# Performance work log

Hardware: AMD Instinct MI355X
Metric: run time of the kernel (lower is better)

The kernel has to match this reference:

```python
import jax, jax.numpy as jnp
import numpy as np

# (C,H,W) of x0..x11; flattened size +1 homogeneous coordinate per key
SHAPES = [(3,32,32),(96,32,32),(96,32,32),(96,16,16),(192,16,16),(192,16,16),(192,8,8),(192,8,8),(192,8,8),(640,1,1),(100,1,1),(10,1,1)]
# (Cin,Cout,k,stride,pad) for conv1..conv9
CONV = [(3,96,3,1,1),(96,96,3,1,1),(96,96,3,2,1),(96,192,3,1,1),(192,192,3,1,1),(192,192,3,2,1),(192,192,3,1,1),(192,192,1,1,0),(192,10,1,1,0)]
B = 128


def setup_inputs():
    key = jax.random.key(0)
    inp = {}
    k, key = jax.random.split(key)
    inp['x0'] = jax.random.normal(k, (int(np.prod(SHAPES[0])) + 1, B), jnp.float32)
    for i, s in enumerate(SHAPES):
        n = int(np.prod(s)) + 1
        k1, k2, key = jax.random.split(key, 3)
        inp['perm%d' % i] = jax.random.permutation(k1, n)
        inp['diag%d' % i] = jax.random.uniform(k2, (n,), jnp.float32, 0.5, 1.5)
    for j, (ci, co, ks, st, pd) in enumerate(CONV):
        k1, k2, key = jax.random.split(key, 3)
        inp['w%d' % (j + 1)] = jax.random.normal(k1, (co, ci, ks, ks), jnp.float32) / np.float32(np.sqrt(ci * ks * ks))
        inp['b%d' % (j + 1)] = jax.random.normal(k2, (co,), jnp.float32) * 0.01
    k1, k2, k3, k4 = jax.random.split(key, 4)
    inp['fw1'] = jax.random.normal(k1, (100, 640), jnp.float32) / np.float32(np.sqrt(640))
    inp['fb1'] = jax.random.normal(k2, (100,), jnp.float32) * 0.01
    inp['fw2'] = jax.random.normal(k3, (10, 100), jnp.float32) / np.float32(np.sqrt(100))
    inp['fb2'] = jax.random.normal(k4, (10,), jnp.float32) * 0.01
    return inp


def _decode(x, perm, diag):
    # A_inv @ x with A_inv = P^T D^{-1}; P^T gather index is argsort(perm)
    return (x / diag[:, None])[jnp.argsort(perm)]


def _encode(y, perm, diag):
    # A @ y with A = D P; (P y)[i] = y[perm[i]]
    return diag[:, None] * y[perm]


def _conv_aug(v, w, b, shape_in, stride, pad):
    # affine-augmented conv: [W b; 0 1] applied to [feat; t]
    C, H, Wd = shape_in
    feat, t = v[:-1], v[-1]                      # (C*H*W, B), (B,)
    x = feat.T.reshape(-1, C, H, Wd)
    y = jax.lax.conv_general_dilated(x, w, (stride, stride), [(pad, pad), (pad, pad)],
                                     dimension_numbers=('NCHW', 'OIHW', 'NCHW'))
    y = y + b[None, :, None, None] * t[:, None, None, None]
    yf = y.reshape(y.shape[0], -1).T             # (N_out, B)
    return jnp.concatenate([yf, t[None, :]], axis=0)


def _fc_aug(v, w, b):
    feat, t = v[:-1], v[-1]
    return jnp.concatenate([w @ feat + b[:, None] * t[None, :], t[None, :]], axis=0)


def _forward(x0, perms, diags, ws, bs, fw1, fb1, fw2, fb2):
    x = x0
    for i in range(9):
        v = _decode(x, perms[i], diags[i])
        y = _conv_aug(v, ws[i], bs[i], SHAPES[i], CONV[i][3], CONV[i][4])
        x = jax.nn.relu(_encode(y, perms[i + 1], diags[i + 1]))
    v = _decode(x, perms[9], diags[9])
    x = jax.nn.relu(_encode(_fc_aug(v, fw1, fb1), perms[10], diags[10]))
    v = _decode(x, perms[10], diags[10])
    return _encode(_fc_aug(v, fw2, fb2), perms[11], diags[11])


def reference(x0, perm0, perm1, perm2, perm3, perm4, perm5, perm6, perm7, perm8, perm9, perm10, perm11,
              diag0, diag1, diag2, diag3, diag4, diag5, diag6, diag7, diag8, diag9, diag10, diag11,
              w1, b1, w2, b2, w3, b3, w4, b4, w5, b5, w6, b6, w7, b7, w8, b8, w9, b9,
              fw1, fb1, fw2, fb2):
    perms = [perm0, perm1, perm2, perm3, perm4, perm5, perm6, perm7, perm8, perm9, perm10, perm11]
    diags = [diag0, diag1, diag2, diag3, diag4, diag5, diag6, diag7, diag8, diag9, diag10, diag11]
    ws = [w1, w2, w3, w4, w5, w6, w7, w8, w9]
    bs = [b1, b2, b3, b4, b5, b6, b7, b8, b9]
    return _forward(x0, perms, diags, ws, bs, fw1, fb1, fw2, fb2)
```

## Files before the change

kernel.cpp:

```cpp
#include <hip/hip_runtime.h>


#define B 128
#define ZPAD 2048

typedef _Float16 f16_t;
typedef __attribute__((ext_vector_type(8))) _Float16 f16x8;
typedef __attribute__((ext_vector_type(4))) _Float16 f16x4;
typedef __attribute__((ext_vector_type(4))) float f32x4;


__global__ void decode_kernel(const float* __restrict__ x, const int* __restrict__ perm,
                              const float* __restrict__ diag, float* __restrict__ v, int nrows) {
    int row = blockIdx.x * 8 + (threadIdx.x >> 5);
    if (row >= nrows) return;
    int lane = threadIdx.x & 31;
    int p = perm[row];
    float inv = 1.0f / diag[row];
    float4 val = ((const float4*)(x + (size_t)row * B))[lane];
    val.x *= inv; val.y *= inv; val.z *= inv; val.w *= inv;
    ((float4*)(v + (size_t)p * B))[lane] = val;
}

__global__ void encode_kernel(const float* __restrict__ y, const int* __restrict__ perm,
                              const float* __restrict__ diag, float* __restrict__ out, int nrows) {
    int row = blockIdx.x * 8 + (threadIdx.x >> 5);
    if (row >= nrows) return;
    int lane = threadIdx.x & 31;
    int p = perm[row];
    float d = diag[row];
    float4 val = ((const float4*)(y + (size_t)p * B))[lane];
    val.x *= d; val.y *= d; val.z *= d; val.w *= d;
    ((float4*)(out + (size_t)row * B))[lane] = val;
}

__global__ void fc_kernel(const float* __restrict__ v, const float* __restrict__ w,
                          const float* __restrict__ b, float* __restrict__ y,
                          int K, int R, int do_relu) {
    int r = blockIdx.x;
    int n = threadIdx.x;
    float t = v[(size_t)K * B + n];
    float val;
    if (r == R) {
        val = t;
    } else {
        float a0 = 0.f, a1 = 0.f, a2 = 0.f, a3 = 0.f;
        float a4 = 0.f, a5 = 0.f, a6 = 0.f, a7 = 0.f;
        const float* wr = w + (size_t)r * K;
        int k = 0;
        for (; k + 8 <= K; k += 8) {
            float4 w0 = *(const float4*)(wr + k);
            float4 w1 = *(const float4*)(wr + k + 4);
            float x0 = v[(size_t)(k + 0) * B + n];
            float x1 = v[(size_t)(k + 1) * B + n];
            float x2 = v[(size_t)(k + 2) * B + n];
            float x3 = v[(size_t)(k + 3) * B + n];
            float x4 = v[(size_t)(k + 4) * B + n];
            float x5 = v[(size_t)(k + 5) * B + n];
            float x6 = v[(size_t)(k + 6) * B + n];
            float x7 = v[(size_t)(k + 7) * B + n];
            a0 = fmaf(w0.x, x0, a0);
            a1 = fmaf(w0.y, x1, a1);
            a2 = fmaf(w0.z, x2, a2);
            a3 = fmaf(w0.w, x3, a3);
            a4 = fmaf(w1.x, x4, a4);
            a5 = fmaf(w1.y, x5, a5);
            a6 = fmaf(w1.z, x6, a6);
            a7 = fmaf(w1.w, x7, a7);
        }
        for (; k < K; ++k)
            a0 = fmaf(wr[k], v[(size_t)k * B + n], a0);
        val = b[r] * t + ((a0 + a1) + (a2 + a3)) + ((a4 + a5) + (a6 + a7));
    }
    if (do_relu) val = fmaxf(val, 0.f);
    y[(size_t)r * B + n] = val;
}


__global__ void pack_input_kernel(const float* __restrict__ v, f16_t* __restrict__ xout,
                                  float* __restrict__ tout) {
    int idx = blockIdx.x * 256 + threadIdx.x;
    int p = idx >> 7, n = idx & 127;
    f16x8 o = {};
    o[0] = (f16_t)v[(size_t)(0 * 1024 + p) * B + n];
    o[1] = (f16_t)v[(size_t)(1 * 1024 + p) * B + n];
    o[2] = (f16_t)v[(size_t)(2 * 1024 + p) * B + n];
    *(f16x8*)(xout + ZPAD + (size_t)p * 1024 + n * 8) = o;
    if (idx < B) tout[idx] = v[(size_t)3072 * B + idx];
}


struct WArgs {
    const float* w[9]; const float* b[9];
    int Ci[9], Co[9], KS[9], Cp[9], NCG[9];
    int woff[10]; int boff[10];
};

__global__ void pack_weights_kernel(WArgs A, f16_t* __restrict__ wp, float* __restrict__ bp,
                                    f16_t* __restrict__ x8a, f16_t* __restrict__ x8b) {
    int idx = blockIdx.x * 256 + threadIdx.x;
    if (idx < ZPAD) { x8a[idx] = (f16_t)0.f; x8b[idx] = (f16_t)0.f; }
    if (idx < A.boff[9]) {
        int l = 0;
        while (idx >= A.boff[l + 1]) ++l;
        int co = idx - A.boff[l];
        bp[idx] = (co < A.Co[l]) ? A.b[l][co] : 0.f;
    }
    if (idx >= A.woff[9]) return;
    int l = 0;
    while (idx >= A.woff[l + 1]) ++l;
    int e = idx - A.woff[l];
    int j = e & 7;
    int t1 = e >> 3;
    int Cp = A.Cp[l];
    int co = t1 % Cp;
    int gg = t1 / Cp;
    int ncg = A.NCG[l];
    int tap = gg / ncg, cg = gg - tap * ncg;
    int ks = A.KS[l];
    int kh = tap / ks, kw = tap - kh * ks;
    int ci = cg * 8 + j;
    float val = 0.f;
    if (co < A.Co[l] && tap < ks * ks && ci < A.Ci[l])
        val = A.w[l][(((size_t)co * A.Ci[l] + ci) * ks + kh) * ks + kw];
    wp[idx] = (f16_t)val;
}


template <int KS, int NS, int NSPLIT, bool F32OUT>
__global__ __launch_bounds__(64) void conv_mfma_kernel(
    const f16_t* __restrict__ xin, const float* __restrict__ t_in,
    const f16_t* __restrict__ wp, const float* __restrict__ bp,
    f16_t* __restrict__ xout, float* __restrict__ t_out, float* __restrict__ f32out,
    int Hi, int Wi, int Wo_log2, int HWo,
    int stride, int pad, int NCG, int nchunk, int KGr, int Co, int Co_pad,
    int PB8, int CB)
{
    constexpr int PF = 2;
    constexpr int MS = 4;
    const int lane = threadIdx.x;
    const int q = lane >> 4;
    const int r = lane & 15;

    const int gb = blockIdx.x;
    const int xcd = gb & 7;
    int j = gb >> 3;
    int nh = 0;
    if (NSPLIT == 2) { nh = j & 1; j >>= 1; }
    const int cog = j % CB;
    const int p   = xcd * PB8 + j / CB;
    const int co0 = cog * 64;
    const int ncol0 = nh * (NS * 16);
    const int ncol8 = ncol0 * 8;

    const int ho = p >> Wo_log2;
    const int wo = p & ((1 << Wo_log2) - 1);
    const f16_t* xdata = xin + ZPAD;

    float tv[NS];
#pragma unroll
    for (int ns = 0; ns < NS; ++ns) tv[ns] = t_in[ncol0 + ns * 16 + r];

    f32x4 acc[MS][NS];
#pragma unroll
    for (int ms = 0; ms < MS; ++ms) {
        float4 b4 = *(const float4*)(bp + co0 + ms * 16 + q * 4);
#pragma unroll
        for (int ns = 0; ns < NS; ++ns) {
            acc[ms][ns][0] = b4.x * tv[ns];
            acc[ms][ns][1] = b4.y * tv[ns];
            acc[ms][ns][2] = b4.z * tv[ns];
            acc[ms][ns][3] = b4.w * tv[ns];
        }
    }

    const int hb = ho * stride - pad, wb = wo * stride - pad;
    const int HiWi = Hi * Wi;
    const int HiWi4 = 4 * HiWi;
    const int NCGHW = NCG * HiWi;
    const int wend = wb + KS;

    int g = q, cg = q, hi = hb, wi = wb, cgHW;
    {
        while (cg >= NCG) { cg -= NCG; ++wi; if (wi == wend) { wi = wb; ++hi; } }
        cgHW = cg * HiWi;
    }

    f16x8 bf[PF][NS], af[PF][MS];

    auto advance = [&]() {
        g += 4; cg += 4; cgHW += HiWi4;
        if (NCG >= 4) {
            int c2 = cg - NCG;
            bool wrap = c2 >= 0;
            int wn = wi + 1;
            bool ww = wrap & (wn == wend);
            cg   = wrap ? c2 : cg;
            cgHW = wrap ? cgHW - NCGHW : cgHW;
            wi   = wrap ? (ww ? wb : wn) : wi;
            hi   = ww ? hi + 1 : hi;
        } else {
            while (cg >= NCG) { cg -= NCG; cgHW -= NCGHW; ++wi; if (wi == wend) { wi = wb; ++hi; } }
        }
    };
    auto loadB = [&](f16x8* b) {
        bool v = (g < KGr) & ((unsigned)hi < (unsigned)Hi) & ((unsigned)wi < (unsigned)Wi);
        int boff = (cgHW + hi * Wi + wi) << 10;
        const f16_t* bb = xdata + (v ? boff : -ZPAD) + ncol8 + r * 8;
#pragma unroll
        for (int ns = 0; ns < NS; ++ns) b[ns] = *(const f16x8*)(bb + ns * 128);
    };
    auto loadA = [&](f16x8* a, int c) {
        int ac = c < nchunk ? c : nchunk - 1;
        const f16_t* ap = wp + (((ac * 4 + q) * Co_pad) + co0 + r) * 8;
#pragma unroll
        for (int ms = 0; ms < MS; ++ms) a[ms] = *(const f16x8*)(ap + ms * 128);
    };
    auto domfma = [&](f16x8* a, f16x8* b) {
#pragma unroll
        for (int ms = 0; ms < MS; ++ms)
#pragma unroll
            for (int ns = 0; ns < NS; ++ns)
                acc[ms][ns] = __builtin_amdgcn_mfma_f32_16x16x32_f16(a[ms], b[ns], acc[ms][ns], 0, 0, 0);
    };

#pragma unroll
    for (int pf = 0; pf < PF; ++pf) { loadB(bf[pf]); loadA(af[pf], pf); advance(); }
    const int nck = ((nchunk + PF - 1) / PF) * PF;
    for (int c = 0; c < nck; c += PF) {
#pragma unroll
        for (int pf = 0; pf < PF; ++pf) {
            domfma(af[pf], bf[pf]);
            loadB(bf[pf]); loadA(af[pf], c + PF + pf); advance();
        }
    }

    if (!F32OUT) {
#pragma unroll
        for (int ms = 0; ms < MS; ++ms) {
            int cob = co0 + ms * 16 + q * 4;
            if (cob < Co) {
                int off0 = ((cob >> 3) * HWo + p) * 1024 + (cob & 7) + ncol8 + r * 8;
#pragma unroll
                for (int ns = 0; ns < NS; ++ns) {
                    f16x4 h;
                    h[0] = (f16_t)fmaxf(acc[ms][ns][0], 0.f);
                    h[1] = (f16_t)fmaxf(acc[ms][ns][1], 0.f);
                    h[2] = (f16_t)fmaxf(acc[ms][ns][2], 0.f);
                    h[3] = (f16_t)fmaxf(acc[ms][ns][3], 0.f);
                    *(f16x4*)(xout + ZPAD + off0 + ns * 128) = h;
                }
            }
        }
        if (gb == 0) {
            t_out[lane]      = fmaxf(t_in[lane], 0.f);
            t_out[lane + 64] = fmaxf(t_in[lane + 64], 0.f);
        }
    } else {
#pragma unroll
        for (int ms = 0; ms < MS; ++ms)
#pragma unroll
            for (int ns = 0; ns < NS; ++ns)
#pragma unroll
                for (int e = 0; e < 4; ++e) {
                    int co = co0 + ms * 16 + q * 4 + e;
                    if (co < Co)
                        f32out[((size_t)co * HWo + p) * B + ncol0 + ns * 16 + r] =
                            fmaxf(acc[ms][ns][e], 0.f);
                }
        if (gb == 0) {
            f32out[(size_t)Co * HWo * B + lane]      = fmaxf(t_in[lane], 0.f);
            f32out[(size_t)Co * HWo * B + lane + 64] = fmaxf(t_in[lane + 64], 0.f);
        }
    }
}


extern "C" void kernel_launch(void* const* d_in, const int* in_sizes, int n_in,
                              void* d_out, int out_size, void* d_ws, size_t ws_size,
                              hipStream_t stream) {
    const float* x0 = (const float*)d_in[0];
    const int*   perm[12];
    const float* diag[12];
    for (int i = 0; i < 12; ++i) {
        perm[i] = (const int*)d_in[1 + 2 * i];
        diag[i] = (const float*)d_in[2 + 2 * i];
    }
    const float* wts[9];
    const float* bia[9];
    for (int j = 0; j < 9; ++j) {
        wts[j] = (const float*)d_in[25 + 2 * j];
        bia[j] = (const float*)d_in[26 + 2 * j];
    }
    const float* fw1 = (const float*)d_in[43];
    const float* fb1 = (const float*)d_in[44];
    const float* fw2 = (const float*)d_in[45];
    const float* fb2 = (const float*)d_in[46];
    float* out = (float*)d_out;

    static const int CiA[9]  = {3, 96, 96, 96, 192, 192, 192, 192, 192};
    static const int CoA[9]  = {96, 96, 96, 192, 192, 192, 192, 192, 10};
    static const int KSA[9]  = {3, 3, 3, 3, 3, 3, 3, 1, 1};
    static const int CpA[9]  = {128, 128, 128, 192, 192, 192, 192, 192, 64};
    static const int NCGA[9] = {1, 12, 12, 12, 24, 24, 24, 24, 24};
    static const int KGRA[9] = {9, 108, 108, 108, 216, 216, 216, 24, 24};
    static const int NCHK[9] = {3, 27, 27, 27, 54, 54, 54, 6, 6};
    static const int HiA[9]  = {32, 32, 32, 16, 16, 16, 8, 8, 8};
    static const int WoL[9]  = {5, 5, 4, 4, 4, 3, 3, 3, 3};
    static const int HWoA[9] = {1024, 1024, 256, 256, 256, 64, 64, 64, 64};
    static const int STA[9]  = {1, 1, 2, 1, 1, 2, 1, 1, 1};
    static const int PDA[9]  = {1, 1, 1, 1, 1, 1, 1, 0, 0};
    static const int NSPL[9] = {1, 1, 1, 1, 1, 2, 2, 2, 2};

    char* wsb = (char*)d_ws;
    const size_t BUF_F32  = 1574912;
    const size_t X8_BYTES = (size_t)(ZPAD + 12 * 1024 * 1024) * 2;
    float* bufA = (float*)wsb;
    float* bufB = (float*)(wsb + BUF_F32);
    f16_t* x8a  = (f16_t*)(wsb + 2 * BUF_F32);
    f16_t* x8b  = (f16_t*)(wsb + 2 * BUF_F32 + X8_BYTES);
    f16_t* wpb  = (f16_t*)(wsb + 2 * BUF_F32 + 2 * X8_BYTES);
    const size_t WP_BYTES = 2888704;
    float* bpb  = (float*)(wsb + 2 * BUF_F32 + 2 * X8_BYTES + WP_BYTES);
    float* t0   = (float*)((char*)bpb + 8192);
    float* t1   = t0 + 256;

    WArgs WA;
    int wo = 0, bo = 0;
    for (int l = 0; l < 9; ++l) {
        WA.w[l] = wts[l]; WA.b[l] = bia[l];
        WA.Ci[l] = CiA[l]; WA.Co[l] = CoA[l]; WA.KS[l] = KSA[l];
        WA.Cp[l] = CpA[l]; WA.NCG[l] = NCGA[l];
        WA.woff[l] = wo; wo += NCHK[l] * 4 * CpA[l] * 8;
        WA.boff[l] = bo; bo += CpA[l];
    }
    WA.woff[9] = wo; WA.boff[9] = bo;
    pack_weights_kernel<<<(wo + 255) / 256, 256, 0, stream>>>(WA, wpb, bpb, x8a, x8b);

    decode_kernel<<<(3073 + 7) / 8, 256, 0, stream>>>(x0, perm[0], diag[0], bufA, 3073);
    pack_input_kernel<<<131072 / 256, 256, 0, stream>>>(bufA, x8a, t0);

    f16_t* xin = x8a; f16_t* xout = x8b;
    float* tin = t0;  float* tout = t1;
    for (int l = 0; l < 9; ++l) {
        const int PB8 = HWoA[l] / 8;
        const int CB = CpA[l] / 64;
        dim3 grid(8 * PB8 * CB * NSPL[l]);
        const f16_t* wpl = wpb + WA.woff[l];
        const float* bpl = bpb + WA.boff[l];
        if (l <= 4) {
            conv_mfma_kernel<3, 8, 1, false><<<grid, 64, 0, stream>>>(
                xin, tin, wpl, bpl, xout, tout, nullptr,
                HiA[l], HiA[l], WoL[l], HWoA[l], STA[l], PDA[l],
                NCGA[l], NCHK[l], KGRA[l], CoA[l], CpA[l], PB8, CB);
        } else if (l <= 6) {
            conv_mfma_kernel<3, 4, 2, false><<<grid, 64, 0, stream>>>(
                xin, tin, wpl, bpl, xout, tout, nullptr,
                HiA[l], HiA[l], WoL[l], HWoA[l], STA[l], PDA[l],
                NCGA[l], NCHK[l], KGRA[l], CoA[l], CpA[l], PB8, CB);
        } else if (l == 7) {
            conv_mfma_kernel<1, 4, 2, false><<<grid, 64, 0, stream>>>(
                xin, tin, wpl, bpl, xout, tout, nullptr,
                HiA[l], HiA[l], WoL[l], HWoA[l], STA[l], PDA[l],
                NCGA[l], NCHK[l], KGRA[l], CoA[l], CpA[l], PB8, CB);
        } else {
            conv_mfma_kernel<1, 4, 2, true><<<grid, 64, 0, stream>>>(
                xin, tin, wpl, bpl, nullptr, nullptr, bufA,
                HiA[l], HiA[l], WoL[l], HWoA[l], STA[l], PDA[l],
                NCGA[l], NCHK[l], KGRA[l], CoA[l], CpA[l], PB8, CB);
        }
        f16_t* xt = xin; xin = xout; xout = xt;
        float* tt = tin; tin = tout; tout = tt;
    }

    fc_kernel<<<101, B, 0, stream>>>(bufA, fw1, fb1, bufB, 640, 100, 1);
    fc_kernel<<<11, B, 0, stream>>>(bufB, fw2, fb2, bufA, 100, 10, 0);
    encode_kernel<<<2, 256, 0, stream>>>(bufA, perm[11], diag[11], out, 11);
}
```

Before: 336.5 us.

## Merge output-channel blocks into multi-wave workgroups and fuse fc2 with encode

For conv layers 1-5, each workgroup now holds one wave per 64-channel output block (2 or 3 waves) covering the same pixel. Before, separate single-wave blocks each handled one channel block. The intent is to share input tile loads across waves through cache and cut the block count. The final FC layer and the encode permutation/scale are also fused into one kernel, which removes one launch and an intermediate buffer round-trip. The trade-off is fewer, larger blocks, which may reduce parallelism on a many-CU GPU.

```diff
diff --git a/kernel.cpp b/kernel.cpp
--- a/kernel.cpp
+++ b/kernel.cpp
@@ -20,18 +20,6 @@
     float4 val = ((const float4*)(x + (size_t)row * B))[lane];
     val.x *= inv; val.y *= inv; val.z *= inv; val.w *= inv;
     ((float4*)(v + (size_t)p * B))[lane] = val;
-}
-
-__global__ void encode_kernel(const float* __restrict__ y, const int* __restrict__ perm,
-                              const float* __restrict__ diag, float* __restrict__ out, int nrows) {
-    int row = blockIdx.x * 8 + (threadIdx.x >> 5);
-    if (row >= nrows) return;
-    int lane = threadIdx.x & 31;
-    int p = perm[row];
-    float d = diag[row];
-    float4 val = ((const float4*)(y + (size_t)p * B))[lane];
-    val.x *= d; val.y *= d; val.z *= d; val.w *= d;
-    ((float4*)(out + (size_t)row * B))[lane] = val;
 }
 
 __global__ void fc_kernel(const float* __restrict__ v, const float* __restrict__ w,
@@ -76,6 +64,32 @@
     y[(size_t)r * B + n] = val;
 }
 
+__global__ void fc2_encode_kernel(const float* __restrict__ v, const float* __restrict__ w,
+                                  const float* __restrict__ b, const int* __restrict__ perm,
+                                  const float* __restrict__ diag, float* __restrict__ out) {
+    int jrow = blockIdx.x;
+    int n = threadIdx.x;
+    int r = perm[jrow];
+    float d = diag[jrow];
+    float t = v[100 * B + n];
+    float val;
+    if (r == 10) {
+        val = t;
+    } else {
+        float a0 = 0.f, a1 = 0.f, a2 = 0.f, a3 = 0.f;
+        const float* wr = w + (size_t)r * 100;
+        for (int k = 0; k < 100; k += 4) {
+            float4 w4 = *(const float4*)(wr + k);
+            a0 = fmaf(w4.x, v[(size_t)(k + 0) * B + n], a0);
+            a1 = fmaf(w4.y, v[(size_t)(k + 1) * B + n], a1);
+            a2 = fmaf(w4.z, v[(size_t)(k + 2) * B + n], a2);
+            a3 = fmaf(w4.w, v[(size_t)(k + 3) * B + n], a3);
+        }
+        val = b[r] * t + (a0 + a1) + (a2 + a3);
+    }
+    out[(size_t)jrow * B + n] = d * val;
+}
+
 
 __global__ void pack_input_kernel(const float* __restrict__ v, f16_t* __restrict__ xout,
                                   float* __restrict__ tout) {
@@ -127,8 +141,8 @@
 }
 
 
-template <int KS, int NS, int NSPLIT, bool F32OUT>
-__global__ __launch_bounds__(64) void conv_mfma_kernel(
+template <int KS, int NS, int NSPLIT, int CBW, bool F32OUT>
+__global__ __launch_bounds__(64 * CBW) void conv_mfma_kernel(
     const f16_t* __restrict__ xin, const float* __restrict__ t_in,
     const f16_t* __restrict__ wp, const float* __restrict__ bp,
     f16_t* __restrict__ xout, float* __restrict__ t_out, float* __restrict__ f32out,
@@ -138,17 +152,23 @@
 {
     constexpr int PF = 2;
     constexpr int MS = 4;
-    const int lane = threadIdx.x;
+    const int wave = threadIdx.x >> 6;
+    const int lane = threadIdx.x & 63;
     const int q = lane >> 4;
     const int r = lane & 15;
 
     const int gb = blockIdx.x;
     const int xcd = gb & 7;
     int j = gb >> 3;
-    int nh = 0;
-    if (NSPLIT == 2) { nh = j & 1; j >>= 1; }
-    const int cog = j % CB;
-    const int p   = xcd * PB8 + j / CB;
+    int nh = 0, cog, p;
+    if (CBW > 1) {
+        cog = wave;
+        p = xcd * PB8 + j;
+    } else {
+        if (NSPLIT == 2) { nh = j & 1; j >>= 1; }
+        cog = j % CB;
+        p = xcd * PB8 + j / CB;
+    }
     const int co0 = cog * 64;
     const int ncol0 = nh * (NS * 16);
     const int ncol8 = ncol0 * 8;
@@ -253,8 +273,8 @@
             }
         }
         if (gb == 0) {
-            t_out[lane]      = fmaxf(t_in[lane], 0.f);
-            t_out[lane + 64] = fmaxf(t_in[lane + 64], 0.f);
+            for (int i = threadIdx.x; i < B; i += CBW * 64)
+                t_out[i] = fmaxf(t_in[i], 0.f);
         }
     } else {
 #pragma unroll
@@ -269,8 +289,8 @@
                             fmaxf(acc[ms][ns][e], 0.f);
                 }
         if (gb == 0) {
-            f32out[(size_t)Co * HWo * B + lane]      = fmaxf(t_in[lane], 0.f);
-            f32out[(size_t)Co * HWo * B + lane + 64] = fmaxf(t_in[lane + 64], 0.f);
+            for (int i = threadIdx.x; i < B; i += CBW * 64)
+                f32out[(size_t)Co * HWo * B + i] = fmaxf(t_in[i], 0.f);
         }
     }
 }
@@ -345,26 +365,30 @@
     for (int l = 0; l < 9; ++l) {
         const int PB8 = HWoA[l] / 8;
         const int CB = CpA[l] / 64;
-        dim3 grid(8 * PB8 * CB * NSPL[l]);
         const f16_t* wpl = wpb + WA.woff[l];
         const float* bpl = bpb + WA.boff[l];
-        if (l <= 4) {
-            conv_mfma_kernel<3, 8, 1, false><<<grid, 64, 0, stream>>>(
+        if (l <= 2) {
+            conv_mfma_kernel<3, 8, 1, 2, false><<<8 * PB8, 128, 0, stream>>>(
+                xin, tin, wpl, bpl, xout, tout, nullptr,
+                HiA[l], HiA[l], WoL[l], HWoA[l], STA[l], PDA[l],
+                NCGA[l], NCHK[l], KGRA[l], CoA[l], CpA[l], PB8, CB);
+        } else if (l <= 4) {
+            conv_mfma_kernel<3, 8, 1, 3, false><<<8 * PB8, 192, 0, stream>>>(
                 xin, tin, wpl, bpl, xout, tout, nullptr,
                 HiA[l], HiA[l], WoL[l], HWoA[l], STA[l], PDA[l],
                 NCGA[l], NCHK[l], KGRA[l], CoA[l], CpA[l], PB8, CB);
         } else if (l <= 6) {
-            conv_mfma_kernel<3, 4, 2, false><<<grid, 64, 0, stream>>>(
+            conv_mfma_kernel<3, 4, 2, 1, false><<<8 * PB8 * CB * 2, 64, 0, stream>>>(
                 xin, tin, wpl, bpl, xout, tout, nullptr,
                 HiA[l], HiA[l], WoL[l], HWoA[l], STA[l], PDA[l],
                 NCGA[l], NCHK[l], KGRA[l], CoA[l], CpA[l], PB8, CB);
         } else if (l == 7) {
-            conv_mfma_kernel<1, 4, 2, false><<<grid, 64, 0, stream>>>(
+            conv_mfma_kernel<1, 4, 2, 1, false><<<8 * PB8 * CB * 2, 64, 0, stream>>>(
                 xin, tin, wpl, bpl, xout, tout, nullptr,
                 HiA[l], HiA[l], WoL[l], HWoA[l], STA[l], PDA[l],
                 NCGA[l], NCHK[l], KGRA[l], CoA[l], CpA[l], PB8, CB);
         } else {
-            conv_mfma_kernel<1, 4, 2, true><<<grid, 64, 0, stream>>>(
+            conv_mfma_kernel<1, 4, 2, 1, true><<<8 * PB8 * CB * 2, 64, 0, stream>>>(
                 xin, tin, wpl, bpl, nullptr, nullptr, bufA,
                 HiA[l], HiA[l], WoL[l], HWoA[l], STA[l], PDA[l],
                 NCGA[l], NCHK[l], KGRA[l], CoA[l], CpA[l], PB8, CB);
@@ -374,6 +398,5 @@
     }
 
     fc_kernel<<<101, B, 0, stream>>>(bufA, fw1, fb1, bufB, 640, 100, 1);
-    fc_kernel<<<11, B, 0, stream>>>(bufB, fw2, fb2, bufA, 100, 10, 0);
-    encode_kernel<<<2, 256, 0, stream>>>(bufA, perm[11], diag[11], out, 11);
-}
+    fc2_encode_kernel<<<11, B, 0, stream>>>(bufB, fw2, fb2, perm[11], diag[11], out);
+}
```

New measurement: 330.3 us. No clear change (-1.8%).
